# Optimization experiments

Measured on AMD Instinct MI355X. Metric: run time of the kernel, lower is better.

Reference implementation:

```python
import jax, jax.numpy as jnp
import numpy as np

NUM_EXPERTS = 64
TOP_K = 2
TEMPERATURE = 1.0
MOMENTUM = 0.9


def _l2norm(x, axis=-1):
    # torch F.normalize: x / max(||x||, eps)
    n = jnp.linalg.norm(x, axis=axis, keepdims=True)
    return x / jnp.maximum(n, 1e-12)


def setup_inputs() -> dict:
    key = jax.random.key(0)
    k1, k2 = jax.random.split(key)
    hidden_states = jax.random.normal(k1, (4, 4096, 2048), dtype=jnp.float32)
    centers = _l2norm(jax.random.normal(k2, (NUM_EXPERTS, 2048), dtype=jnp.float32))
    return {"hidden_states": hidden_states, "centers": centers}


def reference(hidden_states, centers):
    B, T, H = hidden_states.shape
    flat = hidden_states.reshape(-1, H).astype(jnp.float32)  # [N, H]
    N = flat.shape[0]

    # cosine-similarity logits
    reps_n = _l2norm(flat)
    centers_n = _l2norm(centers)
    temp = jnp.maximum(jnp.float32(TEMPERATURE), 1e-6)
    logits = (reps_n @ centers_n.T) / temp  # [N, E]

    probs = jax.nn.softmax(logits, axis=-1)
    top_w, top_ids = jax.lax.top_k(probs, TOP_K)  # [N, k]
    top_w = top_w / (jnp.sum(top_w, axis=-1, keepdims=True) + 1e-9)

    # EMA center update from top-1 routed expert (training+update path)
    route = top_ids[:, 0]  # [N]
    sums = jax.ops.segment_sum(flat, route, num_segments=NUM_EXPERTS)  # [E, H]
    counts = jax.ops.segment_sum(jnp.ones((N, 1), jnp.float32), route,
                                 num_segments=NUM_EXPERTS)  # [E, 1]
    means = sums / (counts + 1e-6)
    updated = _l2norm(MOMENTUM * centers + (1.0 - MOMENTUM) * means)
    new_centers = jnp.where(counts > 0, updated, centers)

    top_ids = top_ids.reshape(B, T, TOP_K)
    top_w = top_w.reshape(B, T, TOP_K)
    return top_ids, top_w, new_centers
```

## Files before the change

### kernel.cpp

```cpp
#include <hip/hip_runtime.h>
#include <math.h>

#define NTOK 16384
#define HDIM 2048
#define NEXP 64
#define KK   32
#define TAU  5e-5f
#define LGT  16384
#define MAXB 2048


__global__ __launch_bounds__(256)
void zero_kernel(float* p, int n) {
  int i = blockIdx.x * 256 + threadIdx.x;
  if (i < n) p[i] = 0.0f;
}

__device__ __forceinline__ float block_reduce_sum(float v, float* red) {
  #pragma unroll
  for (int o = 32; o > 0; o >>= 1) v += __shfl_down(v, o, 64);
  int lane = threadIdx.x & 63;
  int wid  = threadIdx.x >> 6;
  if (lane == 0) red[wid] = v;
  __syncthreads();
  float s = red[0] + red[1] + red[2] + red[3];
  __syncthreads();
  return s;
}

__device__ __forceinline__ double block_reduce_sum_f64(double v, double* red) {
  const int tid = threadIdx.x;
  red[tid] = v;
  __syncthreads();
  if (tid < 128) red[tid] += red[tid + 128];
  __syncthreads();
  if (tid < 64)  red[tid] += red[tid + 64];
  __syncthreads();
  double s = 0.0;
  if (tid < 64) {
    s = red[tid];
    #pragma unroll
    for (int o = 32; o > 0; o >>= 1) s += __shfl_down(s, o, 64);
  }
  if (tid == 0) red[0] = s;
  __syncthreads();
  s = red[0];
  __syncthreads();
  return s;
}

__global__ __launch_bounds__(256)
void cnorm_kernel(const float* __restrict__ c, float* __restrict__ inv_nc) {
  __shared__ float red[4];
  int e = blockIdx.x;
  float ss = 0.f;
  #pragma unroll
  for (int j = 0; j < 8; ++j) {
    float v = c[e * HDIM + threadIdx.x + j * 256];
    ss += v * v;
  }
  float tot = block_reduce_sum(ss, red);
  if (threadIdx.x == 0) inv_nc[e] = 1.0f / fmaxf(sqrtf(tot), 1e-12f);
}

__global__ __launch_bounds__(256)
void cnormalize_kernel(const float* __restrict__ c, float* __restrict__ bn) {
  __shared__ double redd[256];
  __shared__ float s_nc;
  const int e = blockIdx.x;
  const int tid = threadIdx.x;
  const float* cr = c + (size_t)e * HDIM;
  double acc = 0.0;
  #pragma unroll
  for (int i = 0; i < 8; ++i) {
    double v = (double)cr[tid + 256 * i];
    acc += v * v;
  }
  double cn = block_reduce_sum_f64(acc, redd);
  if (tid == 0) s_nc = (float)fmax(sqrt(cn), 1e-12);
  __syncthreads();
  const double nc = (double)s_nc;
  #pragma unroll
  for (int i = 0; i < 8; ++i) {
    int k = tid + 256 * i;
    bn[(size_t)e * HDIM + k] = (float)((double)cr[k] / nc);
  }
}

__global__ __launch_bounds__(256)
void gemm_kernel(const float* __restrict__ x, const float* __restrict__ c,
                 float* __restrict__ logits, float* __restrict__ xnorm2) {
  __shared__ __align__(16) float xs[KK][132];
  __shared__ __align__(16) float cs[KK][68];

  const int tid = threadIdx.x;
  const int mt  = blockIdx.x >> 2;
  const int ks  = blockIdx.x & 3;
  const int t0  = mt * 128;
  const int kb  = ks * 512;
  const int tx  = tid & 15;
  const int ty  = tid >> 4;
  const int r0  = ty * 8;
  const int e0t = tx * 4;
  const int sr = tid >> 1;
  const int sq = (tid & 1) * 16;
  const int er = tid >> 2;
  const int eq = (tid & 3) * 8;

  const float* xrow = x + (size_t)(t0 + sr) * HDIM + kb + sq;
  const float* crow = c + (size_t)er * HDIM + kb + eq;

  float4 xp[4], cp[2];
  #pragma unroll
  for (int i = 0; i < 4; ++i) xp[i] = *(const float4*)(xrow + 4 * i);
  #pragma unroll
  for (int i = 0; i < 2; ++i) cp[i] = *(const float4*)(crow + 4 * i);

  float acc[4][8];
  #pragma unroll
  for (int j = 0; j < 4; ++j)
    #pragma unroll
    for (int i = 0; i < 8; ++i) acc[j][i] = 0.f;
  float nacc = 0.f;

  for (int it = 0; it < 16; ++it) {
    __syncthreads();
    #pragma unroll
    for (int i = 0; i < 4; ++i) {
      xs[sq + 4*i + 0][sr] = xp[i].x; xs[sq + 4*i + 1][sr] = xp[i].y;
      xs[sq + 4*i + 2][sr] = xp[i].z; xs[sq + 4*i + 3][sr] = xp[i].w;
      nacc += xp[i].x*xp[i].x + xp[i].y*xp[i].y + xp[i].z*xp[i].z + xp[i].w*xp[i].w;
    }
    #pragma unroll
    for (int i = 0; i < 2; ++i) {
      cs[eq + 4*i + 0][er] = cp[i].x; cs[eq + 4*i + 1][er] = cp[i].y;
      cs[eq + 4*i + 2][er] = cp[i].z; cs[eq + 4*i + 3][er] = cp[i].w;
    }
    __syncthreads();
    if (it < 15) {
      const float* xn = xrow + (it + 1) * KK;
      const float* cn = crow + (it + 1) * KK;
      #pragma unroll
      for (int i = 0; i < 4; ++i) xp[i] = *(const float4*)(xn + 4 * i);
      #pragma unroll
      for (int i = 0; i < 2; ++i) cp[i] = *(const float4*)(cn + 4 * i);
    }
    #pragma unroll
    for (int k = 0; k < KK; ++k) {
      float4 a0 = *(const float4*)&xs[k][r0];
      float4 a1 = *(const float4*)&xs[k][r0 + 4];
      float4 b  = *(const float4*)&cs[k][e0t];
      acc[0][0] += b.x*a0.x; acc[0][1] += b.x*a0.y; acc[0][2] += b.x*a0.z; acc[0][3] += b.x*a0.w;
      acc[0][4] += b.x*a1.x; acc[0][5] += b.x*a1.y; acc[0][6] += b.x*a1.z; acc[0][7] += b.x*a1.w;
      acc[1][0] += b.y*a0.x; acc[1][1] += b.y*a0.y; acc[1][2] += b.y*a0.z; acc[1][3] += b.y*a0.w;
      acc[1][4] += b.y*a1.x; acc[1][5] += b.y*a1.y; acc[1][6] += b.y*a1.z; acc[1][7] += b.y*a1.w;
      acc[2][0] += b.z*a0.x; acc[2][1] += b.z*a0.y; acc[2][2] += b.z*a0.z; acc[2][3] += b.z*a0.w;
      acc[2][4] += b.z*a1.x; acc[2][5] += b.z*a1.y; acc[2][6] += b.z*a1.z; acc[2][7] += b.z*a1.w;
      acc[3][0] += b.w*a0.x; acc[3][1] += b.w*a0.y; acc[3][2] += b.w*a0.z; acc[3][3] += b.w*a0.w;
      acc[3][4] += b.w*a1.x; acc[3][5] += b.w*a1.y; acc[3][6] += b.w*a1.z; acc[3][7] += b.w*a1.w;
    }
  }

  atomicAdd(&xnorm2[t0 + sr], nacc);

  float* lt = &xs[0][0];
  #pragma unroll
  for (int eh = 0; eh < 2; ++eh) {
    __syncthreads();
    if ((tx >> 3) == eh) {
      const int exl = (tx & 7) * 4;
      #pragma unroll
      for (int j = 0; j < 4; ++j)
        #pragma unroll
        for (int i = 0; i < 8; ++i)
          lt[(exl + j) * 128 + r0 + i] = acc[j][i];
    }
    __syncthreads();
    #pragma unroll
    for (int n = 0; n < 16; ++n) {
      const int f = tid + n * 256;
      const int e = (f >> 7) + eh * 32;
      const int t = f & 127;
      atomicAdd(&logits[(size_t)e * LGT + t0 + t], lt[f]);
    }
  }
}

__global__ __launch_bounds__(256)
void softmax_kernel(const float* __restrict__ logits, const float* __restrict__ xnorm2,
                    const float* __restrict__ inv_nc, float* __restrict__ out,
                    int* __restrict__ route, int* __restrict__ nflag,
                    int* __restrict__ flags) {
  __shared__ float snc[NEXP];
  const int tid = threadIdx.x;
  if (tid < NEXP) snc[tid] = inv_nc[tid];
  __syncthreads();
  const int t = blockIdx.x * 256 + tid;
  const float inv_nx = 1.0f / fmaxf(sqrtf(xnorm2[t]), 1e-12f);
  float lv[NEXP];
  #pragma unroll
  for (int e = 0; e < NEXP; ++e)
    lv[e] = logits[(size_t)e * LGT + t] * snc[e] * inv_nx;
  float m1 = -1e30f, m2 = -1e30f, m3 = -1e30f;
  int i1 = 0, i2 = 0;
  #pragma unroll
  for (int e = 0; e < NEXP; ++e) {
    float l = lv[e];
    if (l > m1)      { m3 = m2; m2 = m1; i2 = i1; m1 = l; i1 = e; }
    else if (l > m2) { m3 = m2; m2 = l; i2 = e; }
    else if (l > m3) { m3 = l; }
  }
  float Z = 0.f;
  #pragma unroll
  for (int e = 0; e < NEXP; ++e) Z += expf(lv[e] - m1);
  const float p1w = 1.0f / Z;
  const float p2w = expf(m2 - m1) / Z;
  const float s   = p1w + p2w + 1e-9f;
  out[t * 2 + 0] = (float)i1;
  out[t * 2 + 1] = (float)i2;
  out[2 * NTOK + t * 2 + 0] = p1w / s;
  out[2 * NTOK + t * 2 + 1] = p2w / s;
  route[t] = i1;
  if ((m1 - m2) < TAU || (m2 - m3) < TAU) {
    int idx = atomicAdd(nflag, 1);
    flags[idx] = t;
  }
}

__global__ __launch_bounds__(256)
void refine_np_kernel(const float* __restrict__ x, const float* __restrict__ bn,
                      float* __restrict__ out, int* __restrict__ route,
                      const int* __restrict__ nflag, const int* __restrict__ flags) {
  __shared__ float a_lds[HDIM];
  __shared__ double redd[256];
  __shared__ float lf[NEXP];
  __shared__ float s_nx;
  const int tid  = threadIdx.x;
  const int lane = tid & 63;
  const int w    = tid >> 6;
  const int n = *nflag;
  for (int j = blockIdx.x; j < n; j += gridDim.x) {
    const int t = flags[j];
    const float* xr = x + (size_t)t * HDIM;
    double xacc = 0.0;
    #pragma unroll
    for (int i = 0; i < 8; ++i) {
      double v = (double)xr[tid + 256 * i];
      xacc += v * v;
    }
    double xn = block_reduce_sum_f64(xacc, redd);
    if (tid == 0) s_nx = (float)fmax(sqrt(xn), 1e-12);
    __syncthreads();
    const double nx = (double)s_nx;
    #pragma unroll
    for (int i = 0; i < 8; ++i) {
      int k = tid + 256 * i;
      a_lds[k] = (float)((double)xr[k] / nx);
    }
    __syncthreads();
    #pragma unroll 1
    for (int ei = 0; ei < 16; ++ei) {
      const int e = w * 16 + ei;
      const float* br = bn + (size_t)e * HDIM;
      double d = 0.0;
      #pragma unroll 8
      for (int i = 0; i < 32; ++i) {
        int k = lane + 64 * i;
        d += (double)a_lds[k] * (double)br[k];
      }
      #pragma unroll
      for (int o = 32; o > 0; o >>= 1) d += __shfl_down(d, o, 64);
      if (lane == 0) lf[e] = (float)d;
    }
    __syncthreads();
    if (tid == 0) {
      float m32 = lf[0];
      for (int ee = 1; ee < NEXP; ++ee) m32 = fmaxf(m32, lf[ee]);
      float ex[NEXP];
      for (int ee = 0; ee < NEXP; ++ee)
        ex[ee] = (float)exp((double)(lf[ee] - m32));
      float r[8];
      #pragma unroll
      for (int q = 0; q < 8; ++q) r[q] = ex[q];
      for (int i = 8; i < NEXP; i += 8)
        #pragma unroll
        for (int q = 0; q < 8; ++q) r[q] += ex[i + q];
      const float Z = ((r[0] + r[1]) + (r[2] + r[3])) + ((r[4] + r[5]) + (r[6] + r[7]));
      float p1 = -1.f, p2 = -1.f;
      int i1 = 0, i2 = 0;
      for (int ee = 0; ee < NEXP; ++ee) {
        float p = ex[ee] / Z;
        if (p > p1)      { p2 = p1; i2 = i1; p1 = p; i1 = ee; }
        else if (p > p2) { p2 = p; i2 = ee; }
      }
      const float s = (p1 + p2) + 1e-9f;
      out[t * 2 + 0] = (float)i1;
      out[t * 2 + 1] = (float)i2;
      out[2 * NTOK + t * 2 + 0] = p1 / s;
      out[2 * NTOK + t * 2 + 1] = p2 / s;
      route[t] = i1;
    }
    __syncthreads();
  }
}

__global__ __launch_bounds__(64)
void refine_np_slow(const float* __restrict__ x, const float* __restrict__ c,
                    float* __restrict__ out, int* __restrict__ route,
                    const int* __restrict__ nflag, const int* __restrict__ flags) {
  __shared__ float lf[NEXP];
  const int e = threadIdx.x;
  const int n = *nflag;
  for (int j = blockIdx.x; j < n; j += gridDim.x) {
    const int t = flags[j];
    const float* xr = x + (size_t)t * HDIM;
    const float* cr = c + (size_t)e * HDIM;
    double xn = 0.0, cn = 0.0;
    for (int k = 0; k < HDIM; ++k) {
      double xv = (double)xr[k];
      double cv = (double)cr[k];
      xn += xv * xv;
      cn += cv * cv;
    }
    const float nx32 = (float)fmax(sqrt(xn), 1e-12);
    const float nc32 = (float)fmax(sqrt(cn), 1e-12);
    double d = 0.0;
    for (int k = 0; k < HDIM; ++k) {
      float a = (float)((double)xr[k] / (double)nx32);
      float b = (float)((double)cr[k] / (double)nc32);
      d += (double)a * (double)b;
    }
    lf[e] = (float)d;
    __syncthreads();
    if (e == 0) {
      float m32 = lf[0];
      for (int ee = 1; ee < NEXP; ++ee) m32 = fmaxf(m32, lf[ee]);
      float ex[NEXP];
      for (int ee = 0; ee < NEXP; ++ee)
        ex[ee] = (float)exp((double)(lf[ee] - m32));
      float r[8];
      #pragma unroll
      for (int q = 0; q < 8; ++q) r[q] = ex[q];
      for (int i = 8; i < NEXP; i += 8)
        #pragma unroll
        for (int q = 0; q < 8; ++q) r[q] += ex[i + q];
      const float Z = ((r[0] + r[1]) + (r[2] + r[3])) + ((r[4] + r[5]) + (r[6] + r[7]));
      float p1 = -1.f, p2 = -1.f;
      int i1 = 0, i2 = 0;
      for (int ee = 0; ee < NEXP; ++ee) {
        float p = ex[ee] / Z;
        if (p > p1)      { p2 = p1; i2 = i1; p1 = p; i1 = ee; }
        else if (p > p2) { p2 = p; i2 = ee; }
      }
      const float s = (p1 + p2) + 1e-9f;
      out[t * 2 + 0] = (float)i1;
      out[t * 2 + 1] = (float)i2;
      out[2 * NTOK + t * 2 + 0] = p1 / s;
      out[2 * NTOK + t * 2 + 1] = p2 / s;
      route[t] = i1;
    }
    __syncthreads();
  }
}

__global__ __launch_bounds__(256)
void scatter_kernel(const int* __restrict__ route, int* __restrict__ cursor,
                    int* __restrict__ bucket) {
  const int t = blockIdx.x * 256 + threadIdx.x;
  const int e = route[t];
  const int pos = atomicAdd(&cursor[e], 1);
  if (pos < MAXB) bucket[e * MAXB + pos] = t;
}

__global__ __launch_bounds__(256)
void segsum_dense(const float* __restrict__ x, const int* __restrict__ cursor,
                  const int* __restrict__ bucket, float* __restrict__ sums) {
  __shared__ int ts[MAXB];
  const int e   = blockIdx.x >> 3;
  const int hc  = blockIdx.x & 7;
  const int hb  = hc * 256;
  const int tid = threadIdx.x;
  int n = cursor[e];
  if (n > MAXB) n = MAXB;
  for (int i = tid; i < n; i += 256) ts[i] = bucket[e * MAXB + i];
  __syncthreads();
  float a[8];
  #pragma unroll
  for (int q = 0; q < 8; ++q) a[q] = 0.f;
  int i = 0;
  for (; i + 7 < n; i += 8) {
    #pragma unroll
    for (int q = 0; q < 8; ++q)
      a[q] += x[(size_t)ts[i + q] * HDIM + hb + tid];
  }
  for (; i < n; ++i) a[0] += x[(size_t)ts[i] * HDIM + hb + tid];
  const float s = ((a[0] + a[1]) + (a[2] + a[3])) + ((a[4] + a[5]) + (a[6] + a[7]));
  sums[e * HDIM + hb + tid] = s;
}

__global__ __launch_bounds__(256)
void finalize_kernel(const float* __restrict__ c, const float* __restrict__ sums,
                     const int* __restrict__ counts, float* __restrict__ out) {
  __shared__ float red[4];
  const int e = blockIdx.x;
  const int tid = threadIdx.x;
  const float cnt = (float)counts[e];
  const float minv = 1.0f / (cnt + 1e-6f);
  float u[8], cv[8];
  float ss = 0.f;
  #pragma unroll
  for (int j = 0; j < 8; ++j) {
    int h = tid + j * 256;
    cv[j] = c[e * HDIM + h];
    float mean = sums[e * HDIM + h] * minv;
    u[j] = 0.9f * cv[j] + 0.1f * mean;
    ss += u[j] * u[j];
  }
  float tot = block_reduce_sum(ss, red);
  float sc = 1.0f / fmaxf(sqrtf(tot), 1e-12f);
  const bool nz = cnt > 0.f;
  #pragma unroll
  for (int j = 0; j < 8; ++j) {
    int h = tid + j * 256;
    out[4 * NTOK + e * HDIM + h] = nz ? u[j] * sc : cv[j];
  }
}

__global__ __launch_bounds__(256)
void router_kernel(const float* __restrict__ x, const float* __restrict__ c,
                   const float* __restrict__ inv_nc, float* __restrict__ out,
                   int* __restrict__ route, int* __restrict__ nflag,
                   int* __restrict__ flags) {
  __shared__ __align__(16) float xs[64][36];
  __shared__ float lgs[64][67];
  const int tid  = threadIdx.x;
  const int lane = tid & 63;
  const int w    = tid >> 6;
  const int t0   = blockIdx.x * 64;
  const int e0   = __builtin_amdgcn_readfirstlane(w * 16);
  const float* cb = c + (size_t)e0 * HDIM;
  const int st = tid >> 3;
  const int sk = (tid & 7) * 4;
  float acc[16];
  #pragma unroll
  for (int e = 0; e < 16; ++e) acc[e] = 0.f;
  float nacc = 0.f;
  float4 p0 = *(const float4*)&x[(size_t)(t0 + st)      * HDIM + sk];
  float4 p1 = *(const float4*)&x[(size_t)(t0 + st + 32) * HDIM + sk];
  for (int k0 = 0; k0 < HDIM; k0 += 32) {
    __syncthreads();
    *(float4*)&xs[st][sk]      = p0;
    *(float4*)&xs[st + 32][sk] = p1;
    __syncthreads();
    const int kn = k0 + 32;
    if (kn < HDIM) {
      p0 = *(const float4*)&x[(size_t)(t0 + st)      * HDIM + kn + sk];
      p1 = *(const float4*)&x[(size_t)(t0 + st + 32) * HDIM + kn + sk];
    }
    float a[32];
    #pragma unroll
    for (int j = 0; j < 32; j += 4) {
      float4 v = *(const float4*)&xs[lane][j];
      a[j] = v.x; a[j+1] = v.y; a[j+2] = v.z; a[j+3] = v.w;
    }
    if (w == 0) {
      #pragma unroll
      for (int j = 0; j < 32; ++j) nacc += a[j] * a[j];
    }
    #pragma unroll
    for (int e = 0; e < 16; ++e) {
      const float* br = cb + (size_t)e * HDIM + k0;
      #pragma unroll
      for (int j = 0; j < 32; j += 4) {
        float4 bv = *(const float4*)&br[j];
        acc[e] += a[j]*bv.x + a[j+1]*bv.y + a[j+2]*bv.z + a[j+3]*bv.w;
      }
    }
  }
  #pragma unroll
  for (int e = 0; e < 16; ++e) lgs[lane][e0 + e] = acc[e] * inv_nc[e0 + e];
  __syncthreads();
  if (w == 0) {
    const float inv_nx = 1.0f / fmaxf(sqrtf(nacc), 1e-12f);
    float m1 = -1e30f, m2 = -1e30f, m3 = -1e30f;
    int i1 = 0, i2 = 0;
    for (int e = 0; e < NEXP; ++e) {
      float l = lgs[lane][e] * inv_nx;
      if (l > m1)      { m3 = m2; m2 = m1; i2 = i1; m1 = l; i1 = e; }
      else if (l > m2) { m3 = m2; m2 = l; i2 = e; }
      else if (l > m3) { m3 = l; }
    }
    float Z = 0.f;
    for (int e = 0; e < NEXP; ++e) Z += expf(lgs[lane][e] * inv_nx - m1);
    const float p1w = 1.0f / Z;
    const float p2w = expf(m2 - m1) / Z;
    const float s   = p1w + p2w + 1e-9f;
    const int tg = t0 + lane;
    out[tg * 2 + 0] = (float)i1;
    out[tg * 2 + 1] = (float)i2;
    out[2 * NTOK + tg * 2 + 0] = p1w / s;
    out[2 * NTOK + tg * 2 + 1] = p2w / s;
    route[tg] = i1;
    if ((m1 - m2) < TAU || (m2 - m3) < TAU) {
      int idx = atomicAdd(nflag, 1);
      flags[idx] = tg;
    }
  }
}

__global__ __launch_bounds__(512)
void segsum_kernel(const float* __restrict__ x, const int* __restrict__ route,
                   float* __restrict__ sums, int* __restrict__ counts) {
  __shared__ float ls[NEXP * 256];
  __shared__ int lcnt[NEXP];
  const int tid  = threadIdx.x;
  const int lane = tid & 63;
  const int w    = tid >> 6;
  const int hc   = blockIdx.x & 7;
  const int tg   = blockIdx.x >> 3;
  const int hb   = hc * 256;
  #pragma unroll
  for (int i = 0; i < 32; ++i) ls[tid + i * 512] = 0.f;
  if (tid < NEXP) lcnt[tid] = 0;
  __syncthreads();
  const int tbase = tg * 512 + w * 64;
  #pragma unroll 4
  for (int i = 0; i < 64; ++i) {
    const int t = tbase + i;
    const int e = route[t];
    const float* xr = x + (size_t)t * HDIM + hb + lane;
    #pragma unroll
    for (int j = 0; j < 4; ++j)
      atomicAdd(&ls[e * 256 + lane + 64 * j], xr[64 * j]);
    if (hc == 0 && lane == 0) atomicAdd(&lcnt[e], 1);
  }
  __syncthreads();
  #pragma unroll
  for (int i = tid; i < NEXP * 256; i += 512) {
    const int e = i >> 8, h = i & 255;
    atomicAdd(&sums[e * HDIM + hb + h], ls[i]);
  }
  if (hc == 0 && tid < NEXP && lcnt[tid] > 0) atomicAdd(&counts[tid], lcnt[tid]);
}

extern "C" void kernel_launch(void* const* d_in, const int* in_sizes, int n_in,
                              void* d_out, int out_size, void* d_ws, size_t ws_size,
                              hipStream_t stream) {
  const float* x = (const float*)d_in[0];
  const float* c = (const float*)d_in[1];
  float* out = (float*)d_out;
  float* ws = (float*)d_ws;

  float* inv_nc = ws;
  int*   counts = (int*)(ws + 64);
  int*   nflag  = (int*)(ws + 128);
  int*   route  = (int*)(ws + 192);
  int*   flags  = (int*)(ws + 16576);
  float* sums   = ws + 32960;
  float* xnorm2 = ws + 164032;
  float* logits = ws + 180416;
  float* bn     = ws + 1228992;
  int*   bucket = (int*)(ws + 1360064);

  const size_t NEED = 1491136ull * 4ull;
  if (ws_size >= NEED) {
    zero_kernel<<<1, 256, 0, stream>>>(ws + 64, 128);
    zero_kernel<<<4160, 256, 0, stream>>>(ws + 164032, 1064960);
    cnorm_kernel<<<NEXP, 256, 0, stream>>>(c, inv_nc);
    cnormalize_kernel<<<NEXP, 256, 0, stream>>>(c, bn);
    gemm_kernel<<<512, 256, 0, stream>>>(x, c, logits, xnorm2);
    softmax_kernel<<<64, 256, 0, stream>>>(logits, xnorm2, inv_nc, out, route, nflag, flags);
    refine_np_kernel<<<512, 256, 0, stream>>>(x, bn, out, route, nflag, flags);
    scatter_kernel<<<64, 256, 0, stream>>>(route, counts, bucket);
    segsum_dense<<<512, 256, 0, stream>>>(x, counts, bucket, sums);
    finalize_kernel<<<NEXP, 256, 0, stream>>>(c, sums, counts, out);
  } else {
    zero_kernel<<<1, 256, 0, stream>>>(ws + 64, 128);
    zero_kernel<<<512, 256, 0, stream>>>(sums, 131072);
    cnorm_kernel<<<NEXP, 256, 0, stream>>>(c, inv_nc);
    router_kernel<<<NTOK / 64, 256, 0, stream>>>(x, c, inv_nc, out, route, nflag, flags);
    refine_np_slow<<<1024, 64, 0, stream>>>(x, c, out, route, nflag, flags);
    segsum_kernel<<<256, 512, 0, stream>>>(x, route, sums, counts);
    finalize_kernel<<<NEXP, 256, 0, stream>>>(c, sums, counts, out);
  }
}
```

Before: 325.2 us.

## Use split-bf16 MFMA for router GEMM and widen softmax grid

Replaces the FP32 FMA register-tiled GEMM with bf16 MFMA instructions. Each float is split into hi and lo bf16 parts, and three products (hh, hl, lh) are accumulated so the result stays close to FP32 accuracy. This moves the logits computation onto the matrix cores and changes the shared-memory layout to K-contiguous padded bf16 tiles. The softmax kernel is relaunched with 64-thread blocks and 256 blocks instead of 64 blocks of 256 threads, to spread tokens across more CUs. The cost is some precision loss from dropping the lo*lo term, which could flip near-tie top-k choices; the existing refine pass may absorb this.

Result: faster. 315.9 us (-2.9%).

```diff
diff --git a/kernel.cpp b/kernel.cpp
--- a/kernel.cpp
+++ b/kernel.cpp
@@ -8,6 +8,12 @@
 #define TAU  5e-5f
 #define LGT  16384
 #define MAXB 2048
+#define KPAD 40
+#define LTS  132
+
+typedef __attribute__((ext_vector_type(8))) short short8;
+typedef __attribute__((ext_vector_type(4))) float f32x4;
+typedef __attribute__((ext_vector_type(2))) unsigned int uint2v;
 
 
 __global__ __launch_bounds__(256)
@@ -87,115 +93,139 @@
   }
 }
 
+__device__ __forceinline__ void cvt2(float v0, float v1, unsigned &hi, unsigned &lo) {
+  unsigned u0 = __float_as_uint(v0);
+  unsigned u1 = __float_as_uint(v1);
+  unsigned h0 = u0 & 0xffff0000u;
+  unsigned h1 = u1 & 0xffff0000u;
+  float r0 = v0 - __uint_as_float(h0);
+  float r1 = v1 - __uint_as_float(h1);
+  hi = (u0 >> 16) | h1;
+  lo = (__float_as_uint(r0) >> 16) | (__float_as_uint(r1) & 0xffff0000u);
+}
+
 __global__ __launch_bounds__(256)
 void gemm_kernel(const float* __restrict__ x, const float* __restrict__ c,
                  float* __restrict__ logits, float* __restrict__ xnorm2) {
-  __shared__ __align__(16) float xs[KK][132];
-  __shared__ __align__(16) float cs[KK][68];
-
-  const int tid = threadIdx.x;
-  const int mt  = blockIdx.x >> 2;
-  const int ks  = blockIdx.x & 3;
-  const int t0  = mt * 128;
-  const int kb  = ks * 512;
-  const int tx  = tid & 15;
-  const int ty  = tid >> 4;
-  const int r0  = ty * 8;
-  const int e0t = tx * 4;
-  const int sr = tid >> 1;
-  const int sq = (tid & 1) * 16;
-  const int er = tid >> 2;
-  const int eq = (tid & 3) * 8;
+  __shared__ __align__(16) unsigned short smem[15360];
+  unsigned short (*Ah)[KPAD] = (unsigned short (*)[KPAD])(smem);
+  unsigned short (*Al)[KPAD] = (unsigned short (*)[KPAD])(smem + 5120);
+  unsigned short (*Bh)[KPAD] = (unsigned short (*)[KPAD])(smem + 10240);
+  unsigned short (*Bl)[KPAD] = (unsigned short (*)[KPAD])(smem + 12800);
+
+  const int tid  = threadIdx.x;
+  const int mt   = blockIdx.x >> 2;
+  const int ks   = blockIdx.x & 3;
+  const int t0   = mt * 128;
+  const int kb   = ks * 512;
+  const int sr   = tid >> 1;
+  const int sq   = (tid & 1) * 16;
+  const int er   = tid >> 2;
+  const int eq   = (tid & 3) * 8;
+  const int lane = tid & 63;
+  const int w    = tid >> 6;
+  const int fr   = lane & 15;
+  const int fk   = (lane >> 4) * 8;
 
   const float* xrow = x + (size_t)(t0 + sr) * HDIM + kb + sq;
   const float* crow = c + (size_t)er * HDIM + kb + eq;
 
-  float4 xp[4], cp[2];
-  #pragma unroll
-  for (int i = 0; i < 4; ++i) xp[i] = *(const float4*)(xrow + 4 * i);
-  #pragma unroll
-  for (int i = 0; i < 2; ++i) cp[i] = *(const float4*)(crow + 4 * i);
-
-  float acc[4][8];
-  #pragma unroll
-  for (int j = 0; j < 4; ++j)
-    #pragma unroll
-    for (int i = 0; i < 8; ++i) acc[j][i] = 0.f;
+  f32x4 xp[4], cp[2];
+  #pragma unroll
+  for (int i = 0; i < 4; ++i) xp[i] = *(const f32x4*)(xrow + 4 * i);
+  #pragma unroll
+  for (int i = 0; i < 2; ++i) cp[i] = *(const f32x4*)(crow + 4 * i);
+
+  f32x4 acc[2][4];
+  #pragma unroll
+  for (int mi = 0; mi < 2; ++mi)
+    #pragma unroll
+    for (int ni = 0; ni < 4; ++ni)
+      acc[mi][ni] = (f32x4){0.f, 0.f, 0.f, 0.f};
   float nacc = 0.f;
 
   for (int it = 0; it < 16; ++it) {
     __syncthreads();
     #pragma unroll
     for (int i = 0; i < 4; ++i) {
-      xs[sq + 4*i + 0][sr] = xp[i].x; xs[sq + 4*i + 1][sr] = xp[i].y;
-      xs[sq + 4*i + 2][sr] = xp[i].z; xs[sq + 4*i + 3][sr] = xp[i].w;
+      unsigned h01, l01, h23, l23;
+      cvt2(xp[i].x, xp[i].y, h01, l01);
+      cvt2(xp[i].z, xp[i].w, h23, l23);
+      *(uint2v*)&Ah[sr][sq + 4 * i] = (uint2v){h01, h23};
+      *(uint2v*)&Al[sr][sq + 4 * i] = (uint2v){l01, l23};
       nacc += xp[i].x*xp[i].x + xp[i].y*xp[i].y + xp[i].z*xp[i].z + xp[i].w*xp[i].w;
     }
     #pragma unroll
     for (int i = 0; i < 2; ++i) {
-      cs[eq + 4*i + 0][er] = cp[i].x; cs[eq + 4*i + 1][er] = cp[i].y;
-      cs[eq + 4*i + 2][er] = cp[i].z; cs[eq + 4*i + 3][er] = cp[i].w;
+      unsigned h01, l01, h23, l23;
+      cvt2(cp[i].x, cp[i].y, h01, l01);
+      cvt2(cp[i].z, cp[i].w, h23, l23);
+      *(uint2v*)&Bh[er][eq + 4 * i] = (uint2v){h01, h23};
+      *(uint2v*)&Bl[er][eq + 4 * i] = (uint2v){l01, l23};
     }
     __syncthreads();
     if (it < 15) {
       const float* xn = xrow + (it + 1) * KK;
       const float* cn = crow + (it + 1) * KK;
       #pragma unroll
-      for (int i = 0; i < 4; ++i) xp[i] = *(const float4*)(xn + 4 * i);
-      #pragma unroll
-      for (int i = 0; i < 2; ++i) cp[i] = *(const float4*)(cn + 4 * i);
-    }
-    #pragma unroll
-    for (int k = 0; k < KK; ++k) {
-      float4 a0 = *(const float4*)&xs[k][r0];
-      float4 a1 = *(const float4*)&xs[k][r0 + 4];
-      float4 b  = *(const float4*)&cs[k][e0t];
-      acc[0][0] += b.x*a0.x; acc[0][1] += b.x*a0.y; acc[0][2] += b.x*a0.z; acc[0][3] += b.x*a0.w;
-      acc[0][4] += b.x*a1.x; acc[0][5] += b.x*a1.y; acc[0][6] += b.x*a1.z; acc[0][7] += b.x*a1.w;
-      acc[1][0] += b.y*a0.x; acc[1][1] += b.y*a0.y; acc[1][2] += b.y*a0.z; acc[1][3] += b.y*a0.w;
-      acc[1][4] += b.y*a1.x; acc[1][5] += b.y*a1.y; acc[1][6] += b.y*a1.z; acc[1][7] += b.y*a1.w;
-      acc[2][0] += b.z*a0.x; acc[2][1] += b.z*a0.y; acc[2][2] += b.z*a0.z; acc[2][3] += b.z*a0.w;
-      acc[2][4] += b.z*a1.x; acc[2][5] += b.z*a1.y; acc[2][6] += b.z*a1.z; acc[2][7] += b.z*a1.w;
-      acc[3][0] += b.w*a0.x; acc[3][1] += b.w*a0.y; acc[3][2] += b.w*a0.z; acc[3][3] += b.w*a0.w;
-      acc[3][4] += b.w*a1.x; acc[3][5] += b.w*a1.y; acc[3][6] += b.w*a1.z; acc[3][7] += b.w*a1.w;
+      for (int i = 0; i < 4; ++i) xp[i] = *(const f32x4*)(xn + 4 * i);
+      #pragma unroll
+      for (int i = 0; i < 2; ++i) cp[i] = *(const f32x4*)(cn + 4 * i);
+    }
+    short8 ah0 = *(const short8*)&Ah[w * 32 + fr][fk];
+    short8 ah1 = *(const short8*)&Ah[w * 32 + 16 + fr][fk];
+    short8 al0 = *(const short8*)&Al[w * 32 + fr][fk];
+    short8 al1 = *(const short8*)&Al[w * 32 + 16 + fr][fk];
+    #pragma unroll
+    for (int ni = 0; ni < 4; ++ni) {
+      short8 bh = *(const short8*)&Bh[ni * 16 + fr][fk];
+      short8 bl = *(const short8*)&Bl[ni * 16 + fr][fk];
+      acc[0][ni] = __builtin_amdgcn_mfma_f32_16x16x32_bf16(ah0, bh, acc[0][ni], 0, 0, 0);
+      acc[0][ni] = __builtin_amdgcn_mfma_f32_16x16x32_bf16(ah0, bl, acc[0][ni], 0, 0, 0);
+      acc[0][ni] = __builtin_amdgcn_mfma_f32_16x16x32_bf16(al0, bh, acc[0][ni], 0, 0, 0);
+      acc[1][ni] = __builtin_amdgcn_mfma_f32_16x16x32_bf16(ah1, bh, acc[1][ni], 0, 0, 0);
+      acc[1][ni] = __builtin_amdgcn_mfma_f32_16x16x32_bf16(ah1, bl, acc[1][ni], 0, 0, 0);
+      acc[1][ni] = __builtin_amdgcn_mfma_f32_16x16x32_bf16(al1, bh, acc[1][ni], 0, 0, 0);
     }
   }
 
   atomicAdd(&xnorm2[t0 + sr], nacc);
 
-  float* lt = &xs[0][0];
+  float* lt = (float*)smem;
   #pragma unroll
   for (int eh = 0; eh < 2; ++eh) {
     __syncthreads();
-    if ((tx >> 3) == eh) {
-      const int exl = (tx & 7) * 4;
-      #pragma unroll
-      for (int j = 0; j < 4; ++j)
-        #pragma unroll
-        for (int i = 0; i < 8; ++i)
-          lt[(exl + j) * 128 + r0 + i] = acc[j][i];
+    #pragma unroll
+    for (int ni2 = 0; ni2 < 2; ++ni2) {
+      const int ni = eh * 2 + ni2;
+      const int e  = ni2 * 16 + fr;
+      #pragma unroll
+      for (int mi = 0; mi < 2; ++mi) {
+        const int t = w * 32 + mi * 16 + (lane >> 4) * 4;
+        *(f32x4*)&lt[e * LTS + t] = acc[mi][ni];
+      }
     }
     __syncthreads();
     #pragma unroll
     for (int n = 0; n < 16; ++n) {
       const int f = tid + n * 256;
-      const int e = (f >> 7) + eh * 32;
+      const int e = f >> 7;
       const int t = f & 127;
-      atomicAdd(&logits[(size_t)e * LGT + t0 + t], lt[f]);
-    }
-  }
-}
-
-__global__ __launch_bounds__(256)
+      atomicAdd(&logits[(size_t)(e + eh * 32) * LGT + t0 + t], lt[e * LTS + t]);
+    }
+  }
+}
+
+__global__ __launch_bounds__(64)
 void softmax_kernel(const float* __restrict__ logits, const float* __restrict__ xnorm2,
                     const float* __restrict__ inv_nc, float* __restrict__ out,
                     int* __restrict__ route, int* __restrict__ nflag,
                     int* __restrict__ flags) {
   __shared__ float snc[NEXP];
   const int tid = threadIdx.x;
-  if (tid < NEXP) snc[tid] = inv_nc[tid];
-  __syncthreads();
-  const int t = blockIdx.x * 256 + tid;
+  snc[tid] = inv_nc[tid];
+  __syncthreads();
+  const int t = blockIdx.x * 64 + tid;
   const float inv_nx = 1.0f / fmaxf(sqrtf(xnorm2[t]), 1e-12f);
   float lv[NEXP];
   #pragma unroll
@@ -569,7 +599,7 @@
     cnorm_kernel<<<NEXP, 256, 0, stream>>>(c, inv_nc);
     cnormalize_kernel<<<NEXP, 256, 0, stream>>>(c, bn);
     gemm_kernel<<<512, 256, 0, stream>>>(x, c, logits, xnorm2);
-    softmax_kernel<<<64, 256, 0, stream>>>(logits, xnorm2, inv_nc, out, route, nflag, flags);
+    softmax_kernel<<<NTOK / 64, 64, 0, stream>>>(logits, xnorm2, inv_nc, out, route, nflag, flags);
     refine_np_kernel<<<512, 256, 0, stream>>>(x, bn, out, route, nflag, flags);
     scatter_kernel<<<64, 256, 0, stream>>>(route, counts, bucket);
     segsum_dense<<<512, 256, 0, stream>>>(x, counts, bucket, sums);
```
